# Performance work log

Measured on AMD Instinct MI355X. Metric: run time of the kernel, lower is better.

Reference implementation:

```python
import jax, jax.numpy as jnp
import numpy as np

N_NODES = 50000
N_EDGES = 600000
D = 128


def setup_inputs() -> dict:
    key = jax.random.key(0)
    k = jax.random.split(key, 6)
    x = jax.random.normal(k[0], (N_NODES, D), dtype=jnp.float32)
    edge_src = jax.random.randint(k[1], (N_EDGES,), 0, N_NODES, dtype=jnp.int64 if jax.config.jax_enable_x64 else jnp.int32)
    edge_dst = jax.random.randint(k[2], (N_EDGES,), 0, N_NODES, dtype=jnp.int64 if jax.config.jax_enable_x64 else jnp.int32)
    # message MLP: [h_src ; h_dst] (2D) -> D, update MLP: [h ; agg] (2D) -> D
    scale = 1.0 / np.sqrt(2 * D)
    W1 = jax.random.normal(k[3], (2 * D, D), dtype=jnp.float32) * scale
    b1 = jnp.zeros((D,), dtype=jnp.float32)
    W2 = jax.random.normal(k[4], (2 * D, D), dtype=jnp.float32) * scale
    b2 = jnp.zeros((D,), dtype=jnp.float32)
    return {"x": x, "edge_src": edge_src, "edge_dst": edge_dst,
            "W1": W1, "b1": b1, "W2": W2, "b2": b2}


def reference(x, edge_src, edge_dst, W1, b1, W2, b2):
    # gather endpoint features per edge: [E, 2D]
    pair = jnp.concatenate([x[edge_src], x[edge_dst]], axis=-1)
    # per-edge message MLP: [E, D]
    msg = jax.nn.relu(pair @ W1 + b1)
    # scatter-aggregate (sum) messages into destination nodes: [N, D]
    agg = jax.ops.segment_sum(msg, edge_dst, num_segments=N_NODES)
    # node update MLP with residual: [N, D]
    upd = jax.nn.relu(jnp.concatenate([x, agg], axis=-1) @ W2 + b2)
    return x + upd
```

## Files before the change

kernel.cpp:

```cpp
#include <hip/hip_runtime.h>
#include <stdint.h>


typedef __attribute__((ext_vector_type(8))) short short8;
typedef __attribute__((ext_vector_type(4))) float floatx4;

#define D 128
#define BSH 6
#define BNODES 64
#define BCAP 1024

static __device__ __forceinline__ unsigned short f2bf(float f) {
    union { float f; unsigned int u; } v; v.f = f;
    unsigned int r = (v.u + 0x7fffu + ((v.u >> 16) & 1u)) >> 16;
    return (unsigned short)r;
}
static __device__ __forceinline__ float bflo(unsigned int u) {
    union { unsigned int u; float f; } v; v.u = u << 16; return v.f;
}
static __device__ __forceinline__ float bfhi(unsigned int u) {
    union { unsigned int u; float f; } v; v.u = u & 0xffff0000u; return v.f;
}

__global__ void k_pre(const float* __restrict__ W1, const float* __restrict__ W2,
                      unsigned short* __restrict__ w1f, unsigned short* __restrict__ w2f,
                      int* __restrict__ bcnt, int N) {
    int gid = blockIdx.x * blockDim.x + threadIdx.x;
    int nb16 = (((N + BNODES - 1) >> BSH) << 4);
    if (gid < nb16) bcnt[gid] = 0;
    if (gid < 32768) {
        int tid = gid;
        int j = tid & 7, lane = (tid >> 3) & 63, ct = (tid >> 9) & 15, kk = tid >> 13;
        int k = kk * 32 + (lane >> 4) * 8 + j;
        int c = ((ct >> 2) << 6) + ((lane & 15) << 2) + (ct & 3);
        float v = (c < 128) ? W1[k * 128 + c] : W1[(128 + k) * 128 + (c - 128)];
        w1f[tid] = f2bf(v);
    } else if (gid < 65536) {
        int tid = gid - 32768;
        int j = tid & 7, lane = (tid >> 3) & 63, ct = (tid >> 9) & 7, kk = tid >> 12;
        int k = kk * 32 + (lane >> 4) * 8 + j;
        int c = ((ct >> 1) << 5) + ((lane & 15) << 1) + (ct & 1);
        w2f[tid] = f2bf(W2[k * 128 + c]);
    }
}

__global__ __launch_bounds__(256, 4) void k_fat1(
    const float* __restrict__ x,
    const unsigned short* __restrict__ w1f,
    const float* __restrict__ b1,
    unsigned short* __restrict__ Ys,
    unsigned short* __restrict__ Yd,
    const int* __restrict__ esrc,
    const int* __restrict__ edst,
    int* __restrict__ bcnt,
    unsigned int* __restrict__ bslot,
    int N, int nTiles, int nb1, int E)
{
    const int tid = threadIdx.x;
    if ((int)blockIdx.x >= nb1) {
        const int hthreads = (gridDim.x - nb1) * 256;
        const int hid = (blockIdx.x - nb1) * 256 + tid;
        const int E4 = E >> 2;
        for (int i = hid; i < E4; i += hthreads) {
            int4 s4 = ((const int4*)esrc)[i];
            int4 d4 = ((const int4*)edst)[i];
            int p;
            p = atomicAdd(&bcnt[(d4.x >> BSH) << 4], 1);
            if (p < BCAP) bslot[((long)(d4.x >> BSH) << 10) + p] =
                ((unsigned int)(d4.x & (BNODES - 1)) << 16) | (unsigned int)s4.x;
            p = atomicAdd(&bcnt[(d4.y >> BSH) << 4], 1);
            if (p < BCAP) bslot[((long)(d4.y >> BSH) << 10) + p] =
                ((unsigned int)(d4.y & (BNODES - 1)) << 16) | (unsigned int)s4.y;
            p = atomicAdd(&bcnt[(d4.z >> BSH) << 4], 1);
            if (p < BCAP) bslot[((long)(d4.z >> BSH) << 10) + p] =
                ((unsigned int)(d4.z & (BNODES - 1)) << 16) | (unsigned int)s4.z;
            p = atomicAdd(&bcnt[(d4.w >> BSH) << 4], 1);
            if (p < BCAP) bslot[((long)(d4.w >> BSH) << 10) + p] =
                ((unsigned int)(d4.w & (BNODES - 1)) << 16) | (unsigned int)s4.w;
        }
        for (int i = (E4 << 2) + hid; i < E; i += hthreads) {
            int d = edst[i];
            int p = atomicAdd(&bcnt[(d >> BSH) << 4], 1);
            if (p < BCAP) bslot[((long)(d >> BSH) << 10) + p] =
                ((unsigned int)(d & (BNODES - 1)) << 16) | (unsigned int)esrc[i];
        }
        return;
    }
    const int w = tid >> 6, lane = tid & 63;
    const int quad = lane >> 4, col = lane & 15;

    short8 wf[4][4];
#pragma unroll
    for (int kk = 0; kk < 4; kk++)
#pragma unroll
        for (int j = 0; j < 4; j++)
            wf[kk][j] = ((const short8*)w1f)[(kk * 16 + w * 4 + j) * 64 + lane];
    float4 bias = make_float4(0.f, 0.f, 0.f, 0.f);
    if (w >= 2) bias = *(const float4*)(b1 + (w - 2) * 64 + col * 4);
    unsigned short* Yhalf = (w < 2) ? Ys : Yd;
    const int cb = (w & 1) * 64;

    for (int t = blockIdx.x; t < nTiles; t += nb1) {
        const int n0 = t * 16;
        const int nr = n0 + col;
        const float* xrow = x + (long)nr * D;
        float4 f[8];
#pragma unroll
        for (int kk = 0; kk < 4; kk++) {
            f[kk * 2]     = *(const float4*)(xrow + kk * 32 + quad * 8);
            f[kk * 2 + 1] = *(const float4*)(xrow + kk * 32 + quad * 8 + 4);
        }
        floatx4 acc[4];
#pragma unroll
        for (int j = 0; j < 4; j++)
#pragma unroll
            for (int q = 0; q < 4; q++) acc[j][q] = 0.f;
#pragma unroll
        for (int kk = 0; kk < 4; kk++) {
            union { short8 s; unsigned int u[4]; } au;
            asm("v_cvt_pk_bf16_f32 %0, %1, %2" : "=v"(au.u[0]) : "v"(f[kk*2].x),   "v"(f[kk*2].y));
            asm("v_cvt_pk_bf16_f32 %0, %1, %2" : "=v"(au.u[1]) : "v"(f[kk*2].z),   "v"(f[kk*2].w));
            asm("v_cvt_pk_bf16_f32 %0, %1, %2" : "=v"(au.u[2]) : "v"(f[kk*2+1].x), "v"(f[kk*2+1].y));
            asm("v_cvt_pk_bf16_f32 %0, %1, %2" : "=v"(au.u[3]) : "v"(f[kk*2+1].z), "v"(f[kk*2+1].w));
#pragma unroll
            for (int j = 0; j < 4; j++)
                acc[j] = __builtin_amdgcn_mfma_f32_16x16x32_bf16(au.s, wf[kk][j], acc[j], 0, 0, 0);
        }
#pragma unroll
        for (int r = 0; r < 4; r++) {
            int n = n0 + quad * 4 + r;
            ushort4 o;
            o.x = f2bf(acc[0][r] + bias.x);
            o.y = f2bf(acc[1][r] + bias.y);
            o.z = f2bf(acc[2][r] + bias.z);
            o.w = f2bf(acc[3][r] + bias.w);
            *(ushort4*)(Yhalf + (long)n * D + cb + col * 4) = o;
        }
    }
}

__global__ __launch_bounds__(512, 2) void k_agg(
    const unsigned short* __restrict__ Ys,
    const unsigned short* __restrict__ Yd,
    const int* __restrict__ bcnt,
    const unsigned int* __restrict__ bslot,
    unsigned short* __restrict__ aggb, int N)
{
    __shared__ unsigned int eb[BCAP];
    __shared__ unsigned short sorted[BCAP];
    __shared__ int cnt64[BNODES], start64[BNODES], cur64[BNODES];
    const int tid = threadIdx.x, w = tid >> 6, lane = tid & 63;
    const int b = blockIdx.x, nb0 = b << BSH;
    int nd = N - nb0; if (nd > BNODES) nd = BNODES;
    int bc = bcnt[b << 4]; if (bc > BCAP) bc = BCAP;

    if (tid < BNODES) cnt64[tid] = 0;
    __syncthreads();
    for (int i = tid; i < bc; i += 512) {
        unsigned int e = bslot[((long)b << 10) + i];
        eb[i] = e;
        atomicAdd(&cnt64[e >> 16], 1);
    }
    __syncthreads();
    if (tid < 64) {
        int c = cnt64[tid];
        int incl = c;
#pragma unroll
        for (int off = 1; off < 64; off <<= 1) {
            int t = __shfl_up(incl, off, 64);
            if (lane >= off) incl += t;
        }
        start64[tid] = incl - c;
        cur64[tid] = incl - c;
    }
    __syncthreads();
    for (int i = tid; i < bc; i += 512) {
        unsigned int e = eb[i];
        int p = atomicAdd(&cur64[e >> 16], 1);
        sorted[p] = (unsigned short)(e & 0xffffu);
    }
    __syncthreads();

    const unsigned short* ysl = Ys + lane * 2;
#pragma unroll
    for (int k = 0; k < 8; k++) {
        int ln = w * 8 + k;
        if (ln >= nd) break;
        const int node = nb0 + ln;
        const int deg = cnt64[ln], base = start64[ln];
        unsigned int ydu = *(const unsigned int*)(Yd + (long)node * D + lane * 2);
        float yd0 = bflo(ydu), yd1 = bfhi(ydu);
        float a0 = 0.f, a1 = 0.f;
        int e = 0;
        for (; e + 8 <= deg; e += 8) {
            int s[8]; unsigned int u[8];
#pragma unroll
            for (int q = 0; q < 8; q++) s[q] = sorted[base + e + q];
#pragma unroll
            for (int q = 0; q < 8; q++) u[q] = *(const unsigned int*)(ysl + (long)s[q] * D);
#pragma unroll
            for (int q = 0; q < 8; q++) {
                a0 += fmaxf(bflo(u[q]) + yd0, 0.f);
                a1 += fmaxf(bfhi(u[q]) + yd1, 0.f);
            }
        }
        for (; e + 4 <= deg; e += 4) {
            int s[4]; unsigned int u[4];
#pragma unroll
            for (int q = 0; q < 4; q++) s[q] = sorted[base + e + q];
#pragma unroll
            for (int q = 0; q < 4; q++) u[q] = *(const unsigned int*)(ysl + (long)s[q] * D);
#pragma unroll
            for (int q = 0; q < 4; q++) {
                a0 += fmaxf(bflo(u[q]) + yd0, 0.f);
                a1 += fmaxf(bfhi(u[q]) + yd1, 0.f);
            }
        }
        for (; e < deg; e++) {
            unsigned int u0 = *(const unsigned int*)(ysl + (long)sorted[base + e] * D);
            a0 += fmaxf(bflo(u0) + yd0, 0.f);
            a1 += fmaxf(bfhi(u0) + yd1, 0.f);
        }
        unsigned int o = (unsigned int)f2bf(a0) | ((unsigned int)f2bf(a1) << 16);
        *(unsigned int*)(aggb + (long)node * D + lane * 2) = o;
    }
}

__global__ __launch_bounds__(256, 4) void k_gemm2(
    const float* __restrict__ x,
    const unsigned short* __restrict__ aggb,
    const unsigned short* __restrict__ w2f,
    const float* __restrict__ b2,
    float* __restrict__ out,
    int N, int nTiles)
{
    const int tid = threadIdx.x, w = tid >> 6, lane = tid & 63;
    const int quad = lane >> 4, col = lane & 15;

    short8 wf[8][2];
#pragma unroll
    for (int kk = 0; kk < 8; kk++)
#pragma unroll
        for (int c = 0; c < 2; c++)
            wf[kk][c] = ((const short8*)w2f)[(kk * 8 + w * 2 + c) * 64 + lane];
    float2 bias = *(const float2*)(b2 + w * 32 + col * 2);

    for (int t = blockIdx.x; t < nTiles; t += gridDim.x) {
        const int n0 = t * 16;
        const int nr = n0 + col;
        const float* xrow = x + (long)nr * D;
        float4 f[8];
        short8 ag[4];
#pragma unroll
        for (int kk = 0; kk < 4; kk++) {
            f[kk * 2]     = *(const float4*)(xrow + kk * 32 + quad * 8);
            f[kk * 2 + 1] = *(const float4*)(xrow + kk * 32 + quad * 8 + 4);
        }
#pragma unroll
        for (int kk = 0; kk < 4; kk++)
            ag[kk] = *(const short8*)(aggb + (long)nr * D + kk * 32 + quad * 8);
        floatx4 acc[2];
#pragma unroll
        for (int c = 0; c < 2; c++)
#pragma unroll
            for (int q = 0; q < 4; q++) acc[c][q] = 0.f;
#pragma unroll
        for (int kk = 0; kk < 4; kk++) {
            union { short8 s; unsigned int u[4]; } au;
            asm("v_cvt_pk_bf16_f32 %0, %1, %2" : "=v"(au.u[0]) : "v"(f[kk*2].x),   "v"(f[kk*2].y));
            asm("v_cvt_pk_bf16_f32 %0, %1, %2" : "=v"(au.u[1]) : "v"(f[kk*2].z),   "v"(f[kk*2].w));
            asm("v_cvt_pk_bf16_f32 %0, %1, %2" : "=v"(au.u[2]) : "v"(f[kk*2+1].x), "v"(f[kk*2+1].y));
            asm("v_cvt_pk_bf16_f32 %0, %1, %2" : "=v"(au.u[3]) : "v"(f[kk*2+1].z), "v"(f[kk*2+1].w));
            acc[0] = __builtin_amdgcn_mfma_f32_16x16x32_bf16(au.s, wf[kk][0], acc[0], 0, 0, 0);
            acc[1] = __builtin_amdgcn_mfma_f32_16x16x32_bf16(au.s, wf[kk][1], acc[1], 0, 0, 0);
        }
#pragma unroll
        for (int kk = 4; kk < 8; kk++) {
            acc[0] = __builtin_amdgcn_mfma_f32_16x16x32_bf16(ag[kk - 4], wf[kk][0], acc[0], 0, 0, 0);
            acc[1] = __builtin_amdgcn_mfma_f32_16x16x32_bf16(ag[kk - 4], wf[kk][1], acc[1], 0, 0, 0);
        }
#pragma unroll
        for (int r = 0; r < 4; r++) {
            int n = n0 + quad * 4 + r;
            long off = (long)n * D + w * 32 + col * 2;
            float2 xr = *(const float2*)(x + off);
            float v0 = fmaxf(acc[0][r] + bias.x, 0.f);
            float v1 = fmaxf(acc[1][r] + bias.y, 0.f);
            *(float2*)(out + off) = make_float2(xr.x + v0, xr.y + v1);
        }
    }
}

extern "C" void kernel_launch(void* const* d_in, const int* in_sizes, int n_in,
                              void* d_out, int out_size, void* d_ws, size_t ws_size,
                              hipStream_t stream)
{
    const float* x   = (const float*)d_in[0];
    const int* esrc  = (const int*)d_in[1];
    const int* edst  = (const int*)d_in[2];
    const float* W1  = (const float*)d_in[3];
    const float* b1  = (const float*)d_in[4];
    const float* W2  = (const float*)d_in[5];
    const float* b2  = (const float*)d_in[6];
    float* out = (float*)d_out;

    const int ND = in_sizes[0];
    const int N  = ND / D;
    const int E  = in_sizes[1];

    char* p = (char*)d_ws;
    auto alloc = [&](size_t bytes) { char* r = p; p += (bytes + 255) & ~(size_t)255; return r; };
    unsigned short* Ys   = (unsigned short*)alloc((size_t)ND * 2);
    unsigned short* Yd   = (unsigned short*)alloc((size_t)ND * 2);
    unsigned short* aggb = (unsigned short*)alloc((size_t)ND * 2);
    unsigned short* w1f  = (unsigned short*)alloc(32768 * 2);
    unsigned short* w2f  = (unsigned short*)alloc(32768 * 2);

    const int NB = (N + BNODES - 1) >> BSH;
    int* bcnt           = (int*)alloc((size_t)NB * 16 * 4);
    unsigned int* bslot = (unsigned int*)alloc((size_t)NB * BCAP * 4);

    const int nTiles = N / 16;
    const int nb1 = (nTiles + 2) / 3;
    const int nbA = ((E >> 2) + 255) / 256;

    k_pre<<<256, 256, 0, stream>>>(W1, W2, w1f, w2f, bcnt, N);
    k_fat1<<<nb1 + nbA, 256, 0, stream>>>(x, w1f, b1, Ys, Yd, esrc, edst, bcnt, bslot,
                                          N, nTiles, nb1, E);
    k_agg<<<NB, 512, 0, stream>>>(Ys, Yd, bcnt, bslot, aggb, N);
    k_gemm2<<<nb1, 256, 0, stream>>>(x, aggb, w2f, b2, out, N, nTiles);
}
```

Measured before the change: 185.6 us.

## Bucket edges with shared-memory histograms per block instead of global atomics

The edge bucketing inside the fused first kernel now uses 64 dedicated blocks, each handling a contiguous edge range. Each block builds a local shared-memory histogram over destination buckets, reserves one range per bucket with a single global atomic, then scatters edges using shared-memory atomics. This replaces one global atomic per edge with far fewer, cutting contention on the bucket counters. The tradeoff is only 64 blocks doing the bucketing serially over about 9.4k edges each, which may lengthen the critical path, and the local arrays are fixed at 1024 buckets, enough for N=50000.

```diff
diff --git a/kernel.cpp b/kernel.cpp
--- a/kernel.cpp
+++ b/kernel.cpp
@@ -9,6 +9,7 @@
 #define BSH 6
 #define BNODES 64
 #define BCAP 1024
+#define NSORT 64
 
 static __device__ __forceinline__ unsigned short f2bf(float f) {
     union { float f; unsigned int u; } v; v.f = f;
@@ -57,31 +58,29 @@
     int N, int nTiles, int nb1, int E)
 {
     const int tid = threadIdx.x;
-    if ((int)blockIdx.x >= nb1) {
-        const int hthreads = (gridDim.x - nb1) * 256;
-        const int hid = (blockIdx.x - nb1) * 256 + tid;
-        const int E4 = E >> 2;
-        for (int i = hid; i < E4; i += hthreads) {
-            int4 s4 = ((const int4*)esrc)[i];
-            int4 d4 = ((const int4*)edst)[i];
-            int p;
-            p = atomicAdd(&bcnt[(d4.x >> BSH) << 4], 1);
-            if (p < BCAP) bslot[((long)(d4.x >> BSH) << 10) + p] =
-                ((unsigned int)(d4.x & (BNODES - 1)) << 16) | (unsigned int)s4.x;
-            p = atomicAdd(&bcnt[(d4.y >> BSH) << 4], 1);
-            if (p < BCAP) bslot[((long)(d4.y >> BSH) << 10) + p] =
-                ((unsigned int)(d4.y & (BNODES - 1)) << 16) | (unsigned int)s4.y;
-            p = atomicAdd(&bcnt[(d4.z >> BSH) << 4], 1);
-            if (p < BCAP) bslot[((long)(d4.z >> BSH) << 10) + p] =
-                ((unsigned int)(d4.z & (BNODES - 1)) << 16) | (unsigned int)s4.z;
-            p = atomicAdd(&bcnt[(d4.w >> BSH) << 4], 1);
-            if (p < BCAP) bslot[((long)(d4.w >> BSH) << 10) + p] =
-                ((unsigned int)(d4.w & (BNODES - 1)) << 16) | (unsigned int)s4.w;
-        }
-        for (int i = (E4 << 2) + hid; i < E; i += hthreads) {
-            int d = edst[i];
-            int p = atomicAdd(&bcnt[(d >> BSH) << 4], 1);
-            if (p < BCAP) bslot[((long)(d >> BSH) << 10) + p] =
+    if ((int)blockIdx.x < NSORT) {
+        __shared__ int lcnt[1024];
+        __shared__ int lbase[1024];
+        const int NB = (N + BNODES - 1) >> BSH;
+        const int eper = (E + NSORT - 1) / NSORT;
+        const int e0 = blockIdx.x * eper;
+        int e1 = e0 + eper; if (e1 > E) e1 = E;
+        for (int i = tid; i < 1024; i += 256) lcnt[i] = 0;
+        __syncthreads();
+        for (int i = e0 + tid; i < e1; i += 256)
+            atomicAdd(&lcnt[edst[i] >> BSH], 1);
+        __syncthreads();
+        for (int c = tid; c < 1024; c += 256) {
+            int lc = lcnt[c];
+            lbase[c] = (lc > 0 && c < NB) ? atomicAdd(&bcnt[c << 4], lc) : 0;
+            lcnt[c] = 0;
+        }
+        __syncthreads();
+        for (int i = e0 + tid; i < e1; i += 256) {
+            int d = edst[i], b = d >> BSH;
+            int lo = atomicAdd(&lcnt[b], 1);
+            int p = lbase[b] + lo;
+            if (p < BCAP) bslot[((long)b << 10) + p] =
                 ((unsigned int)(d & (BNODES - 1)) << 16) | (unsigned int)esrc[i];
         }
         return;
@@ -100,7 +99,7 @@
     unsigned short* Yhalf = (w < 2) ? Ys : Yd;
     const int cb = (w & 1) * 64;
 
-    for (int t = blockIdx.x; t < nTiles; t += nb1) {
+    for (int t = blockIdx.x - NSORT; t < nTiles; t += nb1) {
         const int n0 = t * 16;
         const int nr = n0 + col;
         const float* xrow = x + (long)nr * D;
@@ -322,11 +321,10 @@
 
     const int nTiles = N / 16;
     const int nb1 = (nTiles + 2) / 3;
-    const int nbA = ((E >> 2) + 255) / 256;
 
     k_pre<<<256, 256, 0, stream>>>(W1, W2, w1f, w2f, bcnt, N);
-    k_fat1<<<nb1 + nbA, 256, 0, stream>>>(x, w1f, b1, Ys, Yd, esrc, edst, bcnt, bslot,
-                                          N, nTiles, nb1, E);
+    k_fat1<<<NSORT + nb1, 256, 0, stream>>>(x, w1f, b1, Ys, Yd, esrc, edst, bcnt, bslot,
+                                            N, nTiles, nb1, E);
     k_agg<<<NB, 512, 0, stream>>>(Ys, Yd, bcnt, bslot, aggb, N);
     k_gemm2<<<nb1, 256, 0, stream>>>(x, aggb, w2f, b2, out, N, nTiles);
 }
```

Measured after the change: 184.1 us. About the same (-0.8%).
